# Performance work log

Measured on AMD Instinct MI355X. Metric: run time of the kernel, lower is better.

The kernel has to match this reference:

```python
import jax, jax.numpy as jnp
import numpy as np

EPS = 1e-8  # F.cosine_similarity default eps


def setup_inputs() -> dict:
    key = jax.random.key(0)
    k1, k2, k3, k4 = jax.random.split(key, 4)
    Q, P, E, V = 4096, 16384, 128, 30000
    query = jax.random.randint(k1, (Q,), 0, V, dtype=jnp.int64)
    para = jax.random.randint(k2, (P,), 0, V, dtype=jnp.int64)
    que_embed = jax.random.normal(k3, (Q, E), dtype=jnp.float32)
    para_embed = jax.random.normal(k4, (P, E), dtype=jnp.float32)
    return {"query": query, "para": para, "que_embed": que_embed, "para_embed": para_embed}


def reference(query, para, que_embed, para_embed):
    # xor_matrix[i, j] = 1 if query[i] == para[j] else 0  -> [Q, P] int64
    xor_matrix = (query[:, None] == para[None, :]).astype(jnp.int64)
    # cos_matrix[i, j] = cosine_similarity(que_embed[i], para_embed[j])
    # torch semantics: dot / (max(||q||, eps) * max(||p||, eps))
    q_norm = jnp.maximum(jnp.linalg.norm(que_embed, axis=-1), EPS)   # [Q]
    p_norm = jnp.maximum(jnp.linalg.norm(para_embed, axis=-1), EPS)  # [P]
    dots = jnp.einsum('qe,pe->qp', que_embed, para_embed)            # [Q, P]
    cos_matrix = dots / (q_norm[:, None] * p_norm[None, :])
    return xor_matrix, cos_matrix
```

## Files before the change

### kernel.cpp

```cpp
#include <hip/hip_runtime.h>
#include <stdint.h>

typedef __attribute__((ext_vector_type(8))) short bf16x8;
typedef __attribute__((ext_vector_type(4))) float f32x4;

__device__ __forceinline__ uint32_t f2bf(float f) {
    uint32_t u = __builtin_bit_cast(uint32_t, f);
    u += 0x7fffu + ((u >> 16) & 1u);
    return u >> 16;
}
__device__ __forceinline__ uint32_t pack2(float a, float b) {
    return f2bf(a) | (f2bf(b) << 16);
}

__global__ __launch_bounds__(256) void prep_norms(const float* __restrict__ qe,
                                                  const float* __restrict__ pe,
                                                  float* __restrict__ rq,
                                                  float* __restrict__ rp,
                                                  int Q, int Pn) {
    int gw = (blockIdx.x * 256 + threadIdx.x) >> 6;
    int lane = threadIdx.x & 63;
    if (gw >= Q + Pn) return;
    const float* src = (gw < Q) ? (qe + (size_t)gw * 128) : (pe + (size_t)(gw - Q) * 128);
    float2 v = *(const float2*)(src + lane * 2);
    float s = v.x * v.x + v.y * v.y;
#pragma unroll
    for (int off = 32; off > 0; off >>= 1) s += __shfl_down(s, off, 64);
    if (lane == 0) {
        float r = 1.0f / fmaxf(sqrtf(s), 1e-8f);
        if (gw < Q) rq[gw] = r; else rp[gw - Q] = r;
    }
}

__global__ __launch_bounds__(256) void conv_frag(const float* __restrict__ src,
                                                 unsigned short* __restrict__ dst,
                                                 int ngroups) {
    int t = blockIdx.x * 256 + threadIdx.x;
    if (t >= ngroups * 256) return;
    int g = t >> 8, rem = t & 255;
    int c = rem >> 6, lane = rem & 63;
    int row = g * 16 + (lane & 15);
    int col = c * 32 + ((lane >> 4) << 3);
    const float* s = src + (size_t)row * 128 + col;
    float4 a0 = *(const float4*)s;
    float4 a1 = *(const float4*)(s + 4);
    uint4 pk = { pack2(a0.x, a0.y), pack2(a0.z, a0.w),
                 pack2(a1.x, a1.y), pack2(a1.z, a1.w) };
    *(uint4*)(dst + (size_t)t * 8) = pk;
}

__global__ __launch_bounds__(256) void xor_stream(const int* __restrict__ qid,
                                                  const int* __restrict__ pid,
                                                  float* __restrict__ oxor,
                                                  int Pn_log2_div4) {
    const size_t T = (size_t)blockIdx.x * 256 + threadIdx.x;
    const int q  = (int)(T >> Pn_log2_div4);
    const int pi = ((int)T & ((1 << Pn_log2_div4) - 1)) << 2;
    const int qv = qid[q];
    const int4 pv = *(const int4*)(pid + pi);
    f32x4 x = { pv.x == qv ? 1.f : 0.f, pv.y == qv ? 1.f : 0.f,
                pv.z == qv ? 1.f : 0.f, pv.w == qv ? 1.f : 0.f };
    __builtin_nontemporal_store(x, (f32x4*)(oxor + (T << 2)));
}

#define PBLK 2048

__global__ __launch_bounds__(256, 4) void cos_gemm(
        const unsigned short* __restrict__ Qf, const unsigned short* __restrict__ Pf,
        const float* __restrict__ rq, const float* __restrict__ rp,
        float* __restrict__ ocos, int Pn) {
    __shared__ __align__(16) float scos[4][16][68];

    const int nwg = gridDim.x;
    const int chunk = nwg >> 3;
    const int bid = blockIdx.x;
    const int wg = (bid & 7) * chunk + (bid >> 3);
    const int nPc = Pn / PBLK;
    const int qg = wg / nPc;
    const int pc = wg % nPc;
    const int pblock = pc * PBLK;

    const int t = threadIdx.x;
    const int lane = t & 63;
    const int w = t >> 6;
    const int lq = lane & 15;
    const int g4 = (lane >> 4) << 2;

    bf16x8 af[4];
    const unsigned short* abase = Qf + (size_t)qg * 2048 + lane * 8;
#pragma unroll
    for (int kk = 0; kk < 4; ++kk)
        af[kk] = *(const bf16x8*)(abase + kk * 512);

    const int qrow_base = qg * 16;
    const float rqv = rq[qrow_base + lq];

    const int frow = lane >> 4;
    const int fcol = (lane & 15) * 4;

    for (int fl = 0; fl < PBLK / 256; ++fl) {
        const int pw = pblock + fl * 256 + w * 64;
#pragma unroll
        for (int f = 0; f < 4; ++f) {
            const int p0 = pw + f * 16;
            const unsigned short* bbase = Pf + (size_t)(p0 >> 4) * 2048 + (size_t)lane * 8;
            bf16x8 bfr[4];
#pragma unroll
            for (int kk = 0; kk < 4; ++kk)
                bfr[kk] = *(const bf16x8*)(bbase + kk * 512);
            f32x4 acc = {0.f, 0.f, 0.f, 0.f};
#pragma unroll
            for (int kk = 0; kk < 4; ++kk)
                acc = __builtin_amdgcn_mfma_f32_16x16x32_bf16(bfr[kk], af[kk], acc, 0, 0, 0);
            const float4 rpv = *(const float4*)(rp + p0 + g4);
            f32x4 c4 = { acc[0]*rqv*rpv.x, acc[1]*rqv*rpv.y,
                         acc[2]*rqv*rpv.z, acc[3]*rqv*rpv.w };
            *(f32x4*)&scos[w][lq][f * 16 + g4] = c4;
        }
#pragma unroll
        for (int rr = 0; rr < 4; ++rr) {
            const int row = rr * 4 + frow;
            f32x4 vc = *(const f32x4*)&scos[w][row][fcol];
            __builtin_nontemporal_store(vc,
                (f32x4*)(ocos + (size_t)(qrow_base + row) * Pn + pw + fcol));
        }
    }
}

extern "C" void kernel_launch(void* const* d_in, const int* in_sizes, int n_in,
                              void* d_out, int out_size, void* d_ws, size_t ws_size,
                              hipStream_t stream) {
    const int*   qid = (const int*)d_in[0];
    const int*   pid = (const int*)d_in[1];
    const float* qe  = (const float*)d_in[2];
    const float* pe  = (const float*)d_in[3];
    const int Q  = in_sizes[0];
    const int Pn = in_sizes[1];

    unsigned short* Qf = (unsigned short*)d_ws;
    unsigned short* Pf = Qf + (size_t)Q * 128;
    float* rq = (float*)(Pf + (size_t)Pn * 128);
    float* rp = rq + Q;

    float* oxor = (float*)d_out;
    float* ocos = oxor + (size_t)Q * (size_t)Pn;

    const int qgroups = Q / 16, pgroups = Pn / 16;
    conv_frag<<<qgroups, 256, 0, stream>>>(qe, Qf, qgroups);
    conv_frag<<<pgroups, 256, 0, stream>>>(pe, Pf, pgroups);
    prep_norms<<<(Q + Pn + 3) / 4, 256, 0, stream>>>(qe, pe, rq, rp, Q, Pn);

    int lg = 0; while ((1 << lg) != Pn / 4) ++lg;
    const int nxb = (int)(((size_t)Q * Pn / 4) / 256);
    xor_stream<<<nxb, 256, 0, stream>>>(qid, pid, oxor, lg);

    const int nblocks = (Q / 16) * (Pn / PBLK);
    cos_gemm<<<nblocks, 256, 0, stream>>>(Qf, Pf, rq, rp, ocos, Pn);
}
```

Measured before the change: 131.1 us.

## Fuse prep kernels, grid-stride xor writer, and scalar row stores in cos GEMM

Merges the two bf16 fragment conversion launches and the norm kernel into one prep kernel that computes squared norms from the same loaded values through a shared-memory reduction. This removes two launches and a second read of the embeddings. The xor writer becomes a grid-stride loop over a fixed 2048 blocks instead of one thread per output vector. The cos GEMM epilogue now writes each of the 16 rows as a full 64-float contiguous line with scalar stores rather than 16-byte vector stores covering four rows, which issues more store instructions in exchange for row-contiguous access.

```diff
diff --git a/kernel.cpp b/kernel.cpp
--- a/kernel.cpp
+++ b/kernel.cpp
@@ -13,54 +13,62 @@
     return f2bf(a) | (f2bf(b) << 16);
 }
 
-__global__ __launch_bounds__(256) void prep_norms(const float* __restrict__ qe,
-                                                  const float* __restrict__ pe,
-                                                  float* __restrict__ rq,
-                                                  float* __restrict__ rp,
-                                                  int Q, int Pn) {
-    int gw = (blockIdx.x * 256 + threadIdx.x) >> 6;
-    int lane = threadIdx.x & 63;
-    if (gw >= Q + Pn) return;
-    const float* src = (gw < Q) ? (qe + (size_t)gw * 128) : (pe + (size_t)(gw - Q) * 128);
-    float2 v = *(const float2*)(src + lane * 2);
-    float s = v.x * v.x + v.y * v.y;
-#pragma unroll
-    for (int off = 32; off > 0; off >>= 1) s += __shfl_down(s, off, 64);
-    if (lane == 0) {
-        float r = 1.0f / fmaxf(sqrtf(s), 1e-8f);
-        if (gw < Q) rq[gw] = r; else rp[gw - Q] = r;
-    }
-}
+__global__ __launch_bounds__(256) void prep_all(const float* __restrict__ qe,
+                                                const float* __restrict__ pe,
+                                                unsigned short* __restrict__ Qf,
+                                                unsigned short* __restrict__ Pf,
+                                                float* __restrict__ rq,
+                                                float* __restrict__ rp,
+                                                int qgroups) {
+    __shared__ float part[16][17];
+    const int gi = blockIdx.x;
+    const int rem = threadIdx.x;
+    const bool isQ = gi < qgroups;
+    const int g = isQ ? gi : gi - qgroups;
+    const float* src = isQ ? qe : pe;
+    unsigned short* dst = isQ ? Qf : Pf;
 
-__global__ __launch_bounds__(256) void conv_frag(const float* __restrict__ src,
-                                                 unsigned short* __restrict__ dst,
-                                                 int ngroups) {
-    int t = blockIdx.x * 256 + threadIdx.x;
-    if (t >= ngroups * 256) return;
-    int g = t >> 8, rem = t & 255;
-    int c = rem >> 6, lane = rem & 63;
-    int row = g * 16 + (lane & 15);
-    int col = c * 32 + ((lane >> 4) << 3);
+    const int c = rem >> 6, lane = rem & 63;
+    const int rowl = lane & 15;
+    const int hi = lane >> 4;
+    const int row = g * 16 + rowl;
+    const int col = c * 32 + hi * 8;
     const float* s = src + (size_t)row * 128 + col;
     float4 a0 = *(const float4*)s;
     float4 a1 = *(const float4*)(s + 4);
     uint4 pk = { pack2(a0.x, a0.y), pack2(a0.z, a0.w),
                  pack2(a1.x, a1.y), pack2(a1.z, a1.w) };
-    *(uint4*)(dst + (size_t)t * 8) = pk;
+    *(uint4*)(dst + ((size_t)g * 256 + rem) * 8) = pk;
+
+    float ssq = a0.x*a0.x + a0.y*a0.y + a0.z*a0.z + a0.w*a0.w
+              + a1.x*a1.x + a1.y*a1.y + a1.z*a1.z + a1.w*a1.w;
+    part[rowl][c * 4 + hi] = ssq;
+    __syncthreads();
+    if (rem < 16) {
+        float s16 = 0.f;
+#pragma unroll
+        for (int j = 0; j < 16; ++j) s16 += part[rem][j];
+        float r = 1.0f / fmaxf(sqrtf(s16), 1e-8f);
+        (isQ ? rq : rp)[g * 16 + rem] = r;
+    }
 }
 
 __global__ __launch_bounds__(256) void xor_stream(const int* __restrict__ qid,
                                                   const int* __restrict__ pid,
                                                   float* __restrict__ oxor,
-                                                  int Pn_log2_div4) {
-    const size_t T = (size_t)blockIdx.x * 256 + threadIdx.x;
-    const int q  = (int)(T >> Pn_log2_div4);
-    const int pi = ((int)T & ((1 << Pn_log2_div4) - 1)) << 2;
-    const int qv = qid[q];
-    const int4 pv = *(const int4*)(pid + pi);
-    f32x4 x = { pv.x == qv ? 1.f : 0.f, pv.y == qv ? 1.f : 0.f,
-                pv.z == qv ? 1.f : 0.f, pv.w == qv ? 1.f : 0.f };
-    __builtin_nontemporal_store(x, (f32x4*)(oxor + (T << 2)));
+                                                  int total4, int pmask_log2) {
+    const int stride = gridDim.x * 256;
+    int idx = blockIdx.x * 256 + threadIdx.x;
+    const int pmask = (1 << pmask_log2) - 1;
+    for (; idx < total4; idx += stride) {
+        const int q = idx >> pmask_log2;
+        const int pi = (idx & pmask) << 2;
+        const int qv = qid[q];
+        const int4 pv = *(const int4*)(pid + pi);
+        f32x4 x = { pv.x == qv ? 1.f : 0.f, pv.y == qv ? 1.f : 0.f,
+                    pv.z == qv ? 1.f : 0.f, pv.w == qv ? 1.f : 0.f };
+        __builtin_nontemporal_store(x, (f32x4*)(oxor + ((size_t)idx << 2)));
+    }
 }
 
 #define PBLK 2048
@@ -95,9 +103,6 @@
     const int qrow_base = qg * 16;
     const float rqv = rq[qrow_base + lq];
 
-    const int frow = lane >> 4;
-    const int fcol = (lane & 15) * 4;
-
     for (int fl = 0; fl < PBLK / 256; ++fl) {
         const int pw = pblock + fl * 256 + w * 64;
 #pragma unroll
@@ -118,11 +123,10 @@
             *(f32x4*)&scos[w][lq][f * 16 + g4] = c4;
         }
 #pragma unroll
-        for (int rr = 0; rr < 4; ++rr) {
-            const int row = rr * 4 + frow;
-            f32x4 vc = *(const f32x4*)&scos[w][row][fcol];
+        for (int r = 0; r < 16; ++r) {
+            float vc = scos[w][r][lane];
             __builtin_nontemporal_store(vc,
-                (f32x4*)(ocos + (size_t)(qrow_base + row) * Pn + pw + fcol));
+                ocos + (size_t)(qrow_base + r) * Pn + pw + lane);
         }
     }
 }
@@ -146,13 +150,11 @@
     float* ocos = oxor + (size_t)Q * (size_t)Pn;
 
     const int qgroups = Q / 16, pgroups = Pn / 16;
-    conv_frag<<<qgroups, 256, 0, stream>>>(qe, Qf, qgroups);
-    conv_frag<<<pgroups, 256, 0, stream>>>(pe, Pf, pgroups);
-    prep_norms<<<(Q + Pn + 3) / 4, 256, 0, stream>>>(qe, pe, rq, rp, Q, Pn);
+    prep_all<<<qgroups + pgroups, 256, 0, stream>>>(qe, pe, Qf, Pf, rq, rp, qgroups);
 
     int lg = 0; while ((1 << lg) != Pn / 4) ++lg;
-    const int nxb = (int)(((size_t)Q * Pn / 4) / 256);
-    xor_stream<<<nxb, 256, 0, stream>>>(qid, pid, oxor, lg);
+    const int total4 = (int)((size_t)Q * Pn / 4);
+    xor_stream<<<2048, 256, 0, stream>>>(qid, pid, oxor, total4, lg);
 
     const int nblocks = (Q / 16) * (Pn / PBLK);
     cos_gemm<<<nblocks, 256, 0, stream>>>(Qf, Pf, rq, rp, ocos, Pn);
```

Measured after the change: 127.5 us. 1.03x faster.
